# Kernel tuning notes

Hardware: AMD Instinct MI355X
Metric: run time of the kernel (lower is better)

The kernel has to match this reference:

```python
import jax, jax.numpy as jnp
import numpy as np

B, D, TX, TY = 32, 192, 256, 1024
NEG = -1e9


def setup_inputs() -> dict:
    key = jax.random.key(0)
    k1, k2, k3, k4 = jax.random.split(key, 4)
    x = jax.random.normal(k1, (B, D, TX), jnp.float32)
    y = jax.random.normal(k2, (B, D, TY), jnp.float32)
    # ensure 1 <= x_lens <= TX <= y_lens <= TY so a monotonic path exists
    x_lens = jax.random.randint(k3, (B,), 64, TX + 1, jnp.int32)
    y_lens = jax.random.randint(k4, (B,), 512, TY + 1, jnp.int32)
    return {"x": x, "x_lens": x_lens, "y": y, "y_lens": y_lens}


def _log_prior(x, y):
    # Gaussian log-prior: factor = -0.5 everywhere, so
    # log_prior[b,t,s] = -0.5*sum_d y^2 + sum_d x*y - 0.5*sum_d x^2 + const
    ndim = x.shape[1]
    const = jnp.asarray(-0.5 * np.log(2.0 * np.pi) * ndim, x.dtype)
    y_sq = -0.5 * jnp.sum(y * y, axis=1)            # [B, TY]
    x_sq = -0.5 * jnp.sum(x * x, axis=1)            # [B, TX]
    xy = jnp.einsum('bdt,bds->bts', x, y)           # [B, TX, TY]
    return y_sq[:, None, :] + xy + x_sq[:, :, None] + const


def _maximum_path(log_prior, x_lens, y_lens):
    # Viterbi-style monotonic alignment search (Glow-TTS / VITS maximum_path).
    b, tx, ty = log_prior.shape
    xr = jnp.arange(tx)

    # --- forward DP over mel frames (columns of the (tx, ty) grid) ---
    col0 = jnp.where(xr[None, :] == 0, log_prior[:, :, 0], NEG)  # [B, TX]

    def fwd(prev, inp):
        lp_col, yi = inp                               # lp_col: [B, TX]
        v_cur = jnp.where(xr[None, :] == yi, NEG, prev)
        v_prev = jnp.concatenate(
            [jnp.full((b, 1), NEG, prev.dtype), prev[:, :-1]], axis=1)
        cur = lp_col + jnp.maximum(v_cur, v_prev)
        return cur, cur

    lp_t = jnp.moveaxis(log_prior, 2, 0)               # [TY, B, TX]
    _, cols = jax.lax.scan(fwd, col0, (lp_t[1:], jnp.arange(1, ty)))
    value = jnp.concatenate([col0[None], cols], axis=0)  # [TY, B, TX]

    # value at column y-1 (dummy at y=0, never used for the decision there)
    vprev = jnp.concatenate([value[:1], value[:-1]], axis=0)

    # --- backtrack from (x_lens-1, y_lens-1) down to y=0 ---
    def bwd(index, inp):
        yi, vpc = inp                                  # vpc: [B, TX]
        active = yi < y_lens                           # [B]
        row = jnp.where(active[:, None],
                        jax.nn.one_hot(index, tx, dtype=log_prior.dtype), 0.0)
        vm1 = jnp.take_along_axis(
            vpc, jnp.maximum(index - 1, 0)[:, None], axis=1)[:, 0]
        v0 = jnp.take_along_axis(vpc, index[:, None], axis=1)[:, 0]
        move = (index != 0) & ((index == yi) | (vm1 > v0)) & active
        return index - move.astype(index.dtype), row

    idx0 = x_lens - 1
    _, rows = jax.lax.scan(bwd, idx0, (jnp.arange(ty), vprev), reverse=True)
    return jnp.moveaxis(rows, 0, 2)                    # [B, TX, TY]


def reference(x, x_lens, y, y_lens):
    log_prior = _log_prior(x, y)
    attn = _maximum_path(log_prior, x_lens, y_lens)
    return jax.lax.stop_gradient(attn)
```

## Files before the change

kernel.cpp:

```cpp
#include <hip/hip_runtime.h>
#include <stdint.h>

#define B_  32
#define D_  192
#define TX_ 256
#define TY_ 1024
#define NEGV -1e9f
#define LPCONST ((float)(-176.43619837529715))

__global__ __launch_bounds__(256) void k0_sq(const float* __restrict__ x,
                                             const float* __restrict__ y,
                                             float* __restrict__ xsq,
                                             float* __restrict__ ysq) {
    int gid = blockIdx.x * 256 + threadIdx.x;
    if (gid < B_ * TX_) {
        int b = gid >> 8, t = gid & 255;
        const float* p = x + (size_t)b * D_ * TX_ + t;
        float s = 0.f;
        #pragma unroll 8
        for (int d = 0; d < D_; ++d) { float v = p[(size_t)d * TX_]; s += v * v; }
        xsq[gid] = -0.5f * s;
    } else {
        int g = gid - B_ * TX_;
        int b = g >> 10, t = g & 1023;
        const float* p = y + (size_t)b * D_ * TY_ + t;
        float s = 0.f;
        #pragma unroll 8
        for (int d = 0; d < D_; ++d) { float v = p[(size_t)d * TY_]; s += v * v; }
        ysq[g] = -0.5f * s;
    }
}

#define BT 128
#define BS 128
#define BK 32
__global__ __launch_bounds__(256) void k1_gemm(const float* __restrict__ x,
                                               const float* __restrict__ y,
                                               const float* __restrict__ xsq,
                                               const float* __restrict__ ysq,
                                               float* __restrict__ lp) {
    __shared__ float xs[BK][BT];
    __shared__ float ys[BK][BS];
    const int id = blockIdx.x;
    const int r  = id & 7;
    const int g  = id >> 3;
    const int b  = r + 8 * (g >> 4);
    const int sub = g & 15;
    const int t0 = (sub >> 3) * BT;
    const int s0 = (sub & 7) * BS;
    const int tid = threadIdx.x;
    const int ti = tid & 15;
    const int si = tid >> 4;

    float acc[8][8];
    #pragma unroll
    for (int i = 0; i < 8; ++i)
        #pragma unroll
        for (int j = 0; j < 8; ++j) acc[i][j] = 0.f;

    const float* xg = x + (size_t)b * D_ * TX_ + t0;
    const float* yg = y + (size_t)b * D_ * TY_ + s0;

    for (int k0 = 0; k0 < D_; k0 += BK) {
        #pragma unroll
        for (int i = 0; i < 4; ++i) {
            int f = tid + i * 256;
            int row = f >> 5;
            int col = (f & 31) * 4;
            float4 v = *(const float4*)(xg + (size_t)(k0 + row) * TX_ + col);
            *(float4*)&xs[row][col] = v;
            float4 w = *(const float4*)(yg + (size_t)(k0 + row) * TY_ + col);
            *(float4*)&ys[row][col] = w;
        }
        __syncthreads();
        #pragma unroll
        for (int k = 0; k < BK; ++k) {
            float xr[8], yr[8];
            *(float4*)&xr[0] = *(float4*)&xs[k][ti * 8];
            *(float4*)&xr[4] = *(float4*)&xs[k][ti * 8 + 4];
            *(float4*)&yr[0] = *(float4*)&ys[k][si * 8];
            *(float4*)&yr[4] = *(float4*)&ys[k][si * 8 + 4];
            #pragma unroll
            for (int i = 0; i < 8; ++i)
                #pragma unroll
                for (int j = 0; j < 8; ++j) acc[i][j] += xr[i] * yr[j];
        }
        __syncthreads();
    }

    float xq[8], yq[8];
    *(float4*)&xq[0] = *(const float4*)(xsq + b * TX_ + t0 + ti * 8);
    *(float4*)&xq[4] = *(const float4*)(xsq + b * TX_ + t0 + ti * 8 + 4);
    *(float4*)&yq[0] = *(const float4*)(ysq + b * TY_ + s0 + si * 8);
    *(float4*)&yq[4] = *(const float4*)(ysq + b * TY_ + s0 + si * 8 + 4);

    #pragma unroll
    for (int js = 0; js < 8; ++js) {
        float* op = lp + (size_t)(b * TY_ + s0 + si * 8 + js) * TX_ + t0 + ti * 8;
        float o[8];
        #pragma unroll
        for (int it = 0; it < 8; ++it) {
            float v = yq[js] + acc[it][js];
            v = v + xq[it];
            o[it] = v + LPCONST;
        }
        *(float4*)op       = *(float4*)&o[0];
        *(float4*)(op + 4) = *(float4*)&o[4];
    }
}

__global__ __launch_bounds__(64, 1) void k2_dp(const float* __restrict__ lp,
                                               const int* __restrict__ xlens,
                                               const int* __restrict__ ylens,
                                               unsigned char* __restrict__ path) {
    __shared__ unsigned int RB[TX_][33];
    __shared__ unsigned int PTw[TY_ / 4];
    unsigned char* PT = (unsigned char*)PTw;

    const int b = blockIdx.x;
    const int l = threadIdx.x;
    const int xlen = xlens[b];
    const int ylen = ylens[b];
    const float* base = lp + (size_t)b * TY_ * TX_ + l * 4;
    const int tt0 = l * 4;

#define LDCOL(s) (*(const float4*)(base + (size_t)(((s) < TY_) ? (s) : (TY_ - 1)) * TX_))

#define PROC(s, fv, PRE) {                                              \
    unsigned int sbit = 1u << ((s) & 31);                               \
    bool e0 = false, e1 = false, e2 = false, e3 = false;                \
    if (PRE) { e0 = (tt0 == (s));     e1 = (tt0 + 1 == (s));            \
               e2 = (tt0 + 2 == (s)); e3 = (tt0 + 3 == (s)); }          \
    if ((l != 0) && (e0 || (shv > p0))) rw0 |= sbit;                    \
    if (e1 || (p0 > p1)) rw1 |= sbit;                                   \
    if (e2 || (p1 > p2)) rw2 |= sbit;                                   \
    if (e3 || (p2 > p3)) rw3 |= sbit;                                   \
    float c3 = (fv).w + fmaxf(e3 ? NEGV : p3, p2);                      \
    float nsh = __shfl_up(c3, 1);                                       \
    float c2 = (fv).z + fmaxf(e2 ? NEGV : p2, p1);                      \
    float c1 = (fv).y + fmaxf(e1 ? NEGV : p1, p0);                      \
    float c0 = (fv).x + fmaxf(e0 ? NEGV : p0, (l == 0) ? NEGV : shv);   \
    p0 = c0; p1 = c1; p2 = c2; p3 = c3; shv = nsh;                      \
}

#define FLUSH(w) { RB[tt0][w] = rw0; RB[tt0 + 1][w] = rw1;              \
                   RB[tt0 + 2][w] = rw2; RB[tt0 + 3][w] = rw3;          \
                   rw0 = rw1 = rw2 = rw3 = 0; }

    float4 g[64];
    #pragma unroll
    for (int i = 0; i < 64; ++i) g[i] = LDCOL(i);

    float p0, p1, p2, p3, shv;
    unsigned int rw0 = 0, rw1 = 0, rw2 = 0, rw3 = 0;

    p0 = (l == 0) ? g[0].x : NEGV;
    p1 = NEGV; p2 = NEGV; p3 = NEGV;
    shv = NEGV;
    g[0] = LDCOL(64);

    #pragma unroll
    for (int j = 1; j < 64; ++j) {
        PROC(j, g[j], true)
        g[j] = LDCOL(j + 64);
        if (j == 31 || j == 63) FLUSH(j >> 5)
    }
    #pragma unroll 1
    for (int sb = 64; sb < 256; sb += 64) {
        #pragma unroll
        for (int j = 0; j < 64; ++j) {
            PROC(sb + j, g[j], true)
            g[j] = LDCOL(sb + j + 64);
            if (j == 31 || j == 63) FLUSH((sb + j) >> 5)
        }
    }
    const int send64 = (ylen + 63) & ~63;
    #pragma unroll 1
    for (int sb = 256; sb < send64; sb += 64) {
        #pragma unroll
        for (int j = 0; j < 64; ++j) {
            PROC(sb + j, g[j], false)
            g[j] = LDCOL(sb + j + 64);
            if (j == 31 || j == 63) FLUSH((sb + j) >> 5)
        }
    }
    __syncthreads();

    if (l == 0) {
        int idx = xlen - 1;
        int yi = ylen - 1;
        int w = yi >> 5;
        unsigned int cur = RB[idx][w];
        unsigned int below = (idx > 0) ? RB[idx - 1][w] : 0u;
        while (yi >= 0) {
            unsigned int m = cur & (0xFFFFFFFFu >> (31 - (yi & 31)));
            if (m) {
                int hb = 31 - __clz(m);
                int lo = (w << 5) + hb;
                for (int q = lo; q <= yi; ++q) PT[q] = (unsigned char)idx;
                --idx;
                cur = below;
                below = (idx > 0) ? RB[idx - 1][w] : 0u;
                yi = lo - 1;
                if (yi >= 0 && (yi >> 5) < w) {
                    w = yi >> 5;
                    cur = RB[idx][w];
                    below = (idx > 0) ? RB[idx - 1][w] : 0u;
                }
            } else {
                int lo = w << 5;
                for (int q = lo; q <= yi; ++q) PT[q] = (unsigned char)idx;
                yi = lo - 1;
                if (yi >= 0) {
                    --w;
                    cur = RB[idx][w];
                    below = (idx > 0) ? RB[idx - 1][w] : 0u;
                }
            }
        }
    }
    __syncthreads();
    {
        unsigned int* pd = (unsigned int*)(path + b * TY_);
        #pragma unroll
        for (int k = 0; k < 4; ++k) pd[l + k * 64] = PTw[l + k * 64];
    }
}

__global__ __launch_bounds__(256) void k3_out(const unsigned char* __restrict__ path,
                                              const int* __restrict__ ylens,
                                              float* __restrict__ out) {
    int F = blockIdx.x * 256 + threadIdx.x;
    int yi = (F & 255) * 4;
    int t  = (F >> 8) & 255;
    int b  = F >> 16;
    int ylen = ylens[b];
    unsigned int pw = *(const unsigned int*)(path + b * TY_ + yi);
    float4 v;
    v.x = (((pw      ) & 255u) == (unsigned)t && yi     < ylen) ? 1.f : 0.f;
    v.y = (((pw >>  8) & 255u) == (unsigned)t && yi + 1 < ylen) ? 1.f : 0.f;
    v.z = (((pw >> 16) & 255u) == (unsigned)t && yi + 2 < ylen) ? 1.f : 0.f;
    v.w = (((pw >> 24) & 255u) == (unsigned)t && yi + 3 < ylen) ? 1.f : 0.f;
    ((float4*)out)[F] = v;
}

extern "C" void kernel_launch(void* const* d_in, const int* in_sizes, int n_in,
                              void* d_out, int out_size, void* d_ws, size_t ws_size,
                              hipStream_t stream) {
    const float* x  = (const float*)d_in[0];
    const int*   xl = (const int*)d_in[1];
    const float* y  = (const float*)d_in[2];
    const int*   yl = (const int*)d_in[3];
    float* out = (float*)d_out;

    char* ws = (char*)d_ws;
    float* xsq = (float*)ws;
    float* ysq = (float*)(ws + 32 * 1024);
    unsigned char* path = (unsigned char*)(ws + 160 * 1024);

    float* lp = out;

    k0_sq  <<<160, 256, 0, stream>>>(x, y, xsq, ysq);
    k1_gemm<<<512, 256, 0, stream>>>(x, y, xsq, ysq, lp);
    k2_dp  <<<B_, 64, 0, stream>>>(lp, xl, yl, path);
    k3_out <<<(B_ * TX_ * TY_ / 4) / 256, 256, 0, stream>>>(path, yl, out);
}
```

Before: 185.3 us.

## Split DP kernel into loader waves and compute wave with LDS double buffer

The DP kernel now runs with 256 threads. Three wavefronts stream 32-column chunks of the log-prior into a double-buffered LDS tile using global_load_lds, while one wavefront runs the serial Viterbi recurrence from LDS. This replaces the 64-deep float4 register prefetch, aiming to hide global memory latency and cut register pressure. In exchange it adds a block-wide barrier every 32 columns and LDS read latency on the critical serial chain.

```diff
diff --git a/kernel.cpp b/kernel.cpp
--- a/kernel.cpp
+++ b/kernel.cpp
@@ -109,32 +109,49 @@
     }
 }
 
-__global__ __launch_bounds__(64, 1) void k2_dp(const float* __restrict__ lp,
-                                               const int* __restrict__ xlens,
-                                               const int* __restrict__ ylens,
-                                               unsigned char* __restrict__ path) {
+__device__ __forceinline__ void gload16(const float* gp, float* lp_) {
+    __builtin_amdgcn_global_load_lds(
+        (const __attribute__((address_space(1))) unsigned int*)(gp),
+        (__attribute__((address_space(3))) unsigned int*)(lp_), 16, 0, 0);
+}
+
+__global__ __launch_bounds__(256, 1) void k2_dp(const float* __restrict__ lp,
+                                                const int* __restrict__ xlens,
+                                                const int* __restrict__ ylens,
+                                                unsigned char* __restrict__ path) {
+    __shared__ float colbuf[2][32 * 256];
     __shared__ unsigned int RB[TX_][33];
     __shared__ unsigned int PTw[TY_ / 4];
     unsigned char* PT = (unsigned char*)PTw;
 
-    const int b = blockIdx.x;
-    const int l = threadIdx.x;
+    const int b   = blockIdx.x;
+    const int tid = threadIdx.x;
+    const int w   = tid >> 6;
+    const int l   = tid & 63;
     const int xlen = xlens[b];
     const int ylen = ylens[b];
-    const float* base = lp + (size_t)b * TY_ * TX_ + l * 4;
+    const int nchunk = (ylen + 31) >> 5;
+    const float* lpb = lp + (size_t)b * TY_ * TX_;
     const int tt0 = l * 4;
-
-#define LDCOL(s) (*(const float4*)(base + (size_t)(((s) < TY_) ? (s) : (TY_ - 1)) * TX_))
-
-#define PROC(s, fv, PRE) {                                              \
-    unsigned int sbit = 1u << ((s) & 31);                               \
+    const int l4  = l * 4;
+
+#define LOADCHUNK(kc, bufI) {                                           \
+    for (int c = w - 1; c < 32; c += 3) {                               \
+        int sg = (kc) * 32 + c; if (sg > TY_ - 1) sg = TY_ - 1;         \
+        gload16(lpb + (size_t)sg * TX_ + l4, &colbuf[bufI][c * 256]);   \
+    }                                                                   \
+}
+
+#define COLRD(bufI, j) (*(float4*)&colbuf[bufI][(j) * 256 + l4])
+
+#define PROC2(sv, sbitv, fv, PRE) {                                     \
     bool e0 = false, e1 = false, e2 = false, e3 = false;                \
-    if (PRE) { e0 = (tt0 == (s));     e1 = (tt0 + 1 == (s));            \
-               e2 = (tt0 + 2 == (s)); e3 = (tt0 + 3 == (s)); }          \
-    if ((l != 0) && (e0 || (shv > p0))) rw0 |= sbit;                    \
-    if (e1 || (p0 > p1)) rw1 |= sbit;                                   \
-    if (e2 || (p1 > p2)) rw2 |= sbit;                                   \
-    if (e3 || (p2 > p3)) rw3 |= sbit;                                   \
+    if (PRE) { e0 = (tt0 == (sv));     e1 = (tt0 + 1 == (sv));          \
+               e2 = (tt0 + 2 == (sv)); e3 = (tt0 + 3 == (sv)); }        \
+    if ((l != 0) && (e0 || (shv > p0))) rw0 |= (sbitv);                 \
+    if (e1 || (p0 > p1)) rw1 |= (sbitv);                                \
+    if (e2 || (p1 > p2)) rw2 |= (sbitv);                                \
+    if (e3 || (p2 > p3)) rw3 |= (sbitv);                                \
     float c3 = (fv).w + fmaxf(e3 ? NEGV : p3, p2);                      \
     float nsh = __shfl_up(c3, 1);                                       \
     float c2 = (fv).z + fmaxf(e2 ? NEGV : p2, p1);                      \
@@ -143,88 +160,92 @@
     p0 = c0; p1 = c1; p2 = c2; p3 = c3; shv = nsh;                      \
 }
 
-#define FLUSH(w) { RB[tt0][w] = rw0; RB[tt0 + 1][w] = rw1;              \
-                   RB[tt0 + 2][w] = rw2; RB[tt0 + 3][w] = rw3;          \
-                   rw0 = rw1 = rw2 = rw3 = 0; }
-
-    float4 g[64];
-    #pragma unroll
-    for (int i = 0; i < 64; ++i) g[i] = LDCOL(i);
-
+#define FLUSH(wd) { RB[tt0][wd] = rw0; RB[tt0 + 1][wd] = rw1;           \
+                    RB[tt0 + 2][wd] = rw2; RB[tt0 + 3][wd] = rw3;       \
+                    rw0 = rw1 = rw2 = rw3 = 0; }
+
+    float4 rr[8];
     float p0, p1, p2, p3, shv;
     unsigned int rw0 = 0, rw1 = 0, rw2 = 0, rw3 = 0;
 
-    p0 = (l == 0) ? g[0].x : NEGV;
-    p1 = NEGV; p2 = NEGV; p3 = NEGV;
-    shv = NEGV;
-    g[0] = LDCOL(64);
-
-    #pragma unroll
-    for (int j = 1; j < 64; ++j) {
-        PROC(j, g[j], true)
-        g[j] = LDCOL(j + 64);
-        if (j == 31 || j == 63) FLUSH(j >> 5)
-    }
-    #pragma unroll 1
-    for (int sb = 64; sb < 256; sb += 64) {
-        #pragma unroll
-        for (int j = 0; j < 64; ++j) {
-            PROC(sb + j, g[j], true)
-            g[j] = LDCOL(sb + j + 64);
-            if (j == 31 || j == 63) FLUSH((sb + j) >> 5)
-        }
-    }
-    const int send64 = (ylen + 63) & ~63;
-    #pragma unroll 1
-    for (int sb = 256; sb < send64; sb += 64) {
-        #pragma unroll
-        for (int j = 0; j < 64; ++j) {
-            PROC(sb + j, g[j], false)
-            g[j] = LDCOL(sb + j + 64);
-            if (j == 31 || j == 63) FLUSH((sb + j) >> 5)
-        }
-    }
+    if (w > 0) LOADCHUNK(0, 0)
     __syncthreads();
 
-    if (l == 0) {
+    for (int k = 0; k < nchunk; ++k) {
+        const int cb = k & 1;
+        if (w > 0) {
+            if (k + 1 < nchunk) {
+                if (w == 1) LOADCHUNK(k + 1, cb ^ 1)
+                else if (w == 2) LOADCHUNK(k + 1, cb ^ 1)
+                else LOADCHUNK(k + 1, cb ^ 1)
+            }
+        } else {
+            #pragma unroll
+            for (int j = 0; j < 8; ++j) rr[j] = COLRD(cb, j);
+            if (k == 0) {
+                p0 = (l == 0) ? rr[0].x : NEGV;
+                p1 = NEGV; p2 = NEGV; p3 = NEGV;
+                shv = NEGV;
+                rr[0] = COLRD(0, 8);
+                #pragma unroll
+                for (int j = 1; j < 32; ++j) {
+                    PROC2(j, 1u << j, rr[j & 7], true)
+                    if (j < 24) rr[j & 7] = COLRD(0, j + 8);
+                }
+            } else if (k < 8) {
+                const int s0c = k << 5;
+                #pragma unroll
+                for (int j = 0; j < 32; ++j) {
+                    PROC2(s0c + j, 1u << j, rr[j & 7], true)
+                    if (j < 24) rr[j & 7] = COLRD(cb, j + 8);
+                }
+            } else {
+                #pragma unroll
+                for (int j = 0; j < 32; ++j) {
+                    PROC2(0, 1u << j, rr[j & 7], false)
+                    if (j < 24) rr[j & 7] = COLRD(cb, j + 8);
+                }
+            }
+            FLUSH(k)
+        }
+        __syncthreads();
+    }
+
+    if (tid == 0) {
         int idx = xlen - 1;
         int yi = ylen - 1;
-        int w = yi >> 5;
-        unsigned int cur = RB[idx][w];
-        unsigned int below = (idx > 0) ? RB[idx - 1][w] : 0u;
+        int wd = yi >> 5;
+        unsigned int cur = RB[idx][wd];
+        unsigned int below = (idx > 0) ? RB[idx - 1][wd] : 0u;
         while (yi >= 0) {
             unsigned int m = cur & (0xFFFFFFFFu >> (31 - (yi & 31)));
             if (m) {
                 int hb = 31 - __clz(m);
-                int lo = (w << 5) + hb;
+                int lo = (wd << 5) + hb;
                 for (int q = lo; q <= yi; ++q) PT[q] = (unsigned char)idx;
                 --idx;
                 cur = below;
-                below = (idx > 0) ? RB[idx - 1][w] : 0u;
+                below = (idx > 0) ? RB[idx - 1][wd] : 0u;
                 yi = lo - 1;
-                if (yi >= 0 && (yi >> 5) < w) {
-                    w = yi >> 5;
-                    cur = RB[idx][w];
-                    below = (idx > 0) ? RB[idx - 1][w] : 0u;
+                if (yi >= 0 && (yi >> 5) < wd) {
+                    wd = yi >> 5;
+                    cur = RB[idx][wd];
+                    below = (idx > 0) ? RB[idx - 1][wd] : 0u;
                 }
             } else {
-                int lo = w << 5;
+                int lo = wd << 5;
                 for (int q = lo; q <= yi; ++q) PT[q] = (unsigned char)idx;
                 yi = lo - 1;
                 if (yi >= 0) {
-                    --w;
-                    cur = RB[idx][w];
-                    below = (idx > 0) ? RB[idx - 1][w] : 0u;
+                    --wd;
+                    cur = RB[idx][wd];
+                    below = (idx > 0) ? RB[idx - 1][wd] : 0u;
                 }
             }
         }
     }
     __syncthreads();
-    {
-        unsigned int* pd = (unsigned int*)(path + b * TY_);
-        #pragma unroll
-        for (int k = 0; k < 4; ++k) pd[l + k * 64] = PTw[l + k * 64];
-    }
+    ((unsigned int*)(path + b * TY_))[tid] = PTw[tid];
 }
 
 __global__ __launch_bounds__(256) void k3_out(const unsigned char* __restrict__ path,
@@ -262,6 +283,6 @@
 
     k0_sq  <<<160, 256, 0, stream>>>(x, y, xsq, ysq);
     k1_gemm<<<512, 256, 0, stream>>>(x, y, xsq, ysq, lp);
-    k2_dp  <<<B_, 64, 0, stream>>>(lp, xl, yl, path);
+    k2_dp  <<<B_, 256, 0, stream>>>(lp, xl, yl, path);
     k3_out <<<(B_ * TX_ * TY_ / 4) / 256, 256, 0, stream>>>(path, yl, out);
 }
```

Measured after the change: 187.0 us. Within noise of the previous version (+0.9%).
